# Kernel optimization log

Measured on AMD Instinct MI355X. Metric: run time of the kernel, lower is better.

Reference implementation:

```python
import jax, jax.numpy as jnp
import numpy as np

FP8_E4M3_MAX = 448.0  # torch.finfo(torch.float8_e4m3fn).max
TOKENS, D_IN, D_OUT = 8192, 4096, 4096


def setup_inputs() -> dict:
    key = jax.random.key(0)
    kx, kw, kb = jax.random.split(key, 3)
    x = jax.random.normal(kx, (TOKENS, D_IN), dtype=jnp.float32)
    # frozen bf16-like master weight, quantized to fp8 with per-tensor scale (as in __init__)
    w = jax.random.normal(kw, (D_OUT, D_IN), dtype=jnp.float32) * 0.02
    amax = jnp.abs(w).max()
    weight_scale = jnp.maximum(amax / FP8_E4M3_MAX, 1e-12).reshape(1)
    weight_fp8 = (w / weight_scale).astype(jnp.float8_e4m3fn)
    bias = jax.random.normal(kb, (D_OUT,), dtype=jnp.float32) * 0.01
    return {"x": x, "weight_fp8": weight_fp8, "weight_scale": weight_scale, "bias": bias}


def reference(x, weight_fp8, weight_scale, bias):
    # dequantize fp8 weight to activation dtype, scalar per-tensor scale
    w = weight_fp8.astype(x.dtype) * weight_scale.astype(x.dtype)  # [D_OUT, D_IN]
    return x @ w.T + bias  # [TOKENS, D_OUT]
```

## Files before the change

### kernel.cpp

```cpp
#include <hip/hip_runtime.h>


#define TILE 128
#define BKK  64
#define BM256 256
#define BN256 256

typedef __attribute__((ext_vector_type(8))) __bf16 bfrag8;
typedef __attribute__((ext_vector_type(4))) float  f32x4;
typedef __attribute__((ext_vector_type(8))) short  s8v;

#define GLOBAL_AS(p) ((const __attribute__((address_space(1))) void*)(p))
#define LDS_AS(p)    ((__attribute__((address_space(3))) void*)(p))

__device__ inline unsigned short f2bf(float f) {
    union { float f; unsigned u; } v; v.f = f;
    unsigned r = v.u + 0x7FFFu + ((v.u >> 16) & 1u);
    return (unsigned short)(r >> 16);
}
__device__ inline float bf2f(unsigned short u) {
    union { unsigned u; float f; } v; v.u = ((unsigned)u) << 16;
    return v.f;
}

__device__ inline int detect_w_f32(const void* w) {
    const unsigned short* u = (const unsigned short*)w;
    unsigned nz = 0;
#pragma unroll
    for (int i = 0; i < 64; ++i) nz |= u[2 * i];
    return nz == 0 ? 1 : 0;
}

__global__ void FP8FL_cvt_x(const float* __restrict__ x, short* __restrict__ xb, long n) {
    long i = ((long)blockIdx.x * blockDim.x + threadIdx.x) * 8;
    if (i >= n) return;
    float4 a = *(const float4*)(x + i);
    float4 b = *(const float4*)(x + i + 4);
    s8v r;
    r[0] = (short)f2bf(a.x); r[1] = (short)f2bf(a.y);
    r[2] = (short)f2bf(a.z); r[3] = (short)f2bf(a.w);
    r[4] = (short)f2bf(b.x); r[5] = (short)f2bf(b.y);
    r[6] = (short)f2bf(b.z); r[7] = (short)f2bf(b.w);
    *(s8v*)(xb + i) = r;
}

__global__ void FP8FL_cvt_w(const void* __restrict__ w, short* __restrict__ wb,
                            const float* __restrict__ scale_p, long n) {
    __shared__ int sdt;
    if (threadIdx.x == 0) sdt = detect_w_f32(w);
    __syncthreads();
    long i = ((long)blockIdx.x * blockDim.x + threadIdx.x) * 8;
    if (i >= n) return;
    const float s = scale_p[0];
    s8v r;
    if (sdt) {
        const float* wf = (const float*)w;
        float4 a = *(const float4*)(wf + i);
        float4 b = *(const float4*)(wf + i + 4);
        r[0] = (short)f2bf(a.x * s); r[1] = (short)f2bf(a.y * s);
        r[2] = (short)f2bf(a.z * s); r[3] = (short)f2bf(a.w * s);
        r[4] = (short)f2bf(b.x * s); r[5] = (short)f2bf(b.y * s);
        r[6] = (short)f2bf(b.z * s); r[7] = (short)f2bf(b.w * s);
    } else {
        const unsigned short* wu = (const unsigned short*)w;
        s8v v = *(const s8v*)(wu + i);
#pragma unroll
        for (int j = 0; j < 8; ++j)
            r[j] = (short)f2bf(bf2f((unsigned short)v[j]) * s);
    }
    *(s8v*)(wb + i) = r;
}

__device__ inline void stage_pair256(const short* __restrict__ A, const short* __restrict__ B,
                                     long row0, long col0, int K, int kc,
                                     char* __restrict__ lds, int d, int p,
                                     int wid, int lane) {
    char* Asl = lds + d * 65536 + p * 16384;
    char* Bsl = lds + d * 65536 + 32768 + p * 16384;
#pragma unroll
    for (int i = 0; i < 2; ++i) {
        int pc = i * 512 + wid * 64 + lane;
        int r  = pc >> 2;
        int j  = (pc & 3) ^ ((r >> 1) & 3);
        const short* ga = A + (size_t)(row0 + r) * K + kc + j * 8;
        const short* gb = B + (size_t)(col0 + r) * K + kc + j * 8;
        char* da = Asl + (i * 512 + wid * 64) * 16;
        char* db = Bsl + (i * 512 + wid * 64) * 16;
        __builtin_amdgcn_global_load_lds(GLOBAL_AS(ga), LDS_AS(da), 16, 0, 0);
        __builtin_amdgcn_global_load_lds(GLOBAL_AS(gb), LDS_AS(db), 16, 0, 0);
    }
}

__global__ __launch_bounds__(512, 2)
void FP8FL_gemm256(const short* __restrict__ A, const short* __restrict__ B,
                   const float* __restrict__ bias, float* __restrict__ C,
                   int M, int N, int K) {
    __shared__ char lds[131072];

    const int tid  = threadIdx.x;
    const int lane = tid & 63;
    const int wid  = tid >> 6;

    const int nwg = gridDim.x;
    const int bid = blockIdx.x;
    const int wg  = (nwg % 8 == 0) ? (bid % 8) * (nwg / 8) + (bid / 8) : bid;

    const int tiles_n = N / BN256;
    const long row0 = (long)(wg / tiles_n) * BM256;
    const long col0 = (long)(wg % tiles_n) * BN256;

    const int wm = wid >> 2, wn = wid & 3;
    const int rl = lane & 15, g = lane >> 4;

    f32x4 acc[8][4];
#pragma unroll
    for (int m = 0; m < 8; ++m)
#pragma unroll
        for (int n = 0; n < 4; ++n) acc[m][n] = (f32x4){0.f, 0.f, 0.f, 0.f};

    const int NT = K / BKK;

    stage_pair256(A, B, row0, col0, K, 0,  lds, 0, 0, wid, lane);
    stage_pair256(A, B, row0, col0, K, 32, lds, 0, 1, wid, lane);
    asm volatile("s_waitcnt vmcnt(4)" ::: "memory");
    __builtin_amdgcn_s_barrier();

    for (int t = 0; t < NT; ++t) {
        const int d = t & 1;
#pragma unroll
        for (int p = 0; p < 2; ++p) {
            const char* Asl = lds + d * 65536 + p * 16384;
            const char* Bsl = lds + d * 65536 + 32768 + p * 16384;
            bfrag8 af[8], bfv[4];
#pragma unroll
            for (int m = 0; m < 8; ++m) {
                int r  = wm * 128 + m * 16 + rl;
                int sl = g ^ ((r >> 1) & 3);
                af[m] = *(const bfrag8*)(Asl + (r * 4 + sl) * 16);
            }
#pragma unroll
            for (int n = 0; n < 4; ++n) {
                int r  = wn * 64 + n * 16 + rl;
                int sl = g ^ ((r >> 1) & 3);
                bfv[n] = *(const bfrag8*)(Bsl + (r * 4 + sl) * 16);
            }
            if (t + 1 < NT)
                stage_pair256(A, B, row0, col0, K, (t + 1) * BKK + p * 32,
                              lds, d ^ 1, p, wid, lane);

            __builtin_amdgcn_s_barrier();
            asm volatile("s_waitcnt lgkmcnt(0)" ::: "memory");
            __builtin_amdgcn_sched_barrier(0);
            __builtin_amdgcn_s_setprio(1);
#pragma unroll
            for (int m = 0; m < 8; ++m)
#pragma unroll
                for (int n = 0; n < 4; ++n)
                    acc[m][n] = __builtin_amdgcn_mfma_f32_16x16x32_bf16(af[m], bfv[n], acc[m][n], 0, 0, 0);
            __builtin_amdgcn_s_setprio(0);

            if (t + 1 < NT)      asm volatile("s_waitcnt vmcnt(4)" ::: "memory");
            else if (p == 0)     asm volatile("s_waitcnt vmcnt(0)" ::: "memory");
            __builtin_amdgcn_s_barrier();
        }
    }

    float bv[4];
#pragma unroll
    for (int n = 0; n < 4; ++n) bv[n] = bias[col0 + wn * 64 + n * 16 + rl];
#pragma unroll
    for (int m = 0; m < 8; ++m) {
#pragma unroll
        for (int jj = 0; jj < 4; ++jj) {
            long r = row0 + wm * 128 + m * 16 + g * 4 + jj;
            float* cp = C + r * (long)N + col0 + wn * 64 + rl;
#pragma unroll
            for (int n = 0; n < 4; ++n) cp[n * 16] = acc[m][n][jj] + bv[n];
        }
    }
}

__global__ void FP8FL_gemm(const short* __restrict__ A, const short* __restrict__ B,
                           const float* __restrict__ bias, float* __restrict__ C,
                           int M, int N, int K) {
    __shared__ short As[TILE * BKK];
    __shared__ short Bs[TILE * BKK];

    const int tid  = threadIdx.x;
    const int lane = tid & 63;
    const int wid  = tid >> 6;

    const int nwg = gridDim.x;
    const int bid = blockIdx.x;
    const int wg  = (nwg % 8 == 0) ? (bid % 8) * (nwg / 8) + (bid / 8) : bid;

    const int tiles_n = N / TILE;
    const int tm = wg / tiles_n, tn = wg % tiles_n;
    const long row0 = (long)tm * TILE;
    const long col0 = (long)tn * TILE;

    const int wm = wid >> 1, wn = wid & 1;

    f32x4 acc[4][4];
#pragma unroll
    for (int i = 0; i < 4; ++i)
#pragma unroll
        for (int j = 0; j < 4; ++j) acc[i][j] = (f32x4){0.f, 0.f, 0.f, 0.f};

    const int rl = lane & 15;
    const int g  = lane >> 4;

    for (int k0 = 0; k0 < K; k0 += BKK) {
        __syncthreads();
#pragma unroll
        for (int i = 0; i < 4; ++i) {
            int c  = i * 256 + tid;
            int r  = c >> 3;
            int ls = c & 7;
            const short* ga = A + ((size_t)(row0 + r) * K + k0 + ls * 8);
            const short* gb = B + ((size_t)(col0 + r) * K + k0 + ls * 8);
            int ldsoff = (i * 256 + wid * 64) * 16;
            __builtin_amdgcn_global_load_lds(GLOBAL_AS(ga), LDS_AS((char*)As + ldsoff), 16, 0, 0);
            __builtin_amdgcn_global_load_lds(GLOBAL_AS(gb), LDS_AS((char*)Bs + ldsoff), 16, 0, 0);
        }
        __syncthreads();

#pragma unroll
        for (int kk = 0; kk < 2; ++kk) {
            bfrag8 af[4], bfr[4];
            const int lsk = kk * 4 + g;
#pragma unroll
            for (int m = 0; m < 4; ++m) {
                int r  = wm * 64 + m * 16 + rl;
                af[m] = *(const bfrag8*)&As[r * 64 + lsk * 8];
            }
#pragma unroll
            for (int n = 0; n < 4; ++n) {
                int r  = wn * 64 + n * 16 + rl;
                bfr[n] = *(const bfrag8*)&Bs[r * 64 + lsk * 8];
            }
#pragma unroll
            for (int m = 0; m < 4; ++m)
#pragma unroll
                for (int n = 0; n < 4; ++n)
                    acc[m][n] = __builtin_amdgcn_mfma_f32_16x16x32_bf16(af[m], bfr[n], acc[m][n], 0, 0, 0);
        }
    }

    float bv[4];
#pragma unroll
    for (int n = 0; n < 4; ++n) bv[n] = bias[col0 + wn * 64 + n * 16 + rl];
#pragma unroll
    for (int m = 0; m < 4; ++m) {
#pragma unroll
        for (int j = 0; j < 4; ++j) {
            long r = row0 + wm * 64 + m * 16 + g * 4 + j;
            float* cp = C + r * (long)N + col0 + wn * 64 + rl;
#pragma unroll
            for (int n = 0; n < 4; ++n) cp[n * 16] = acc[m][n][j] + bv[n];
        }
    }
}

__global__ void FP8FL_gemm_fused(const float* __restrict__ X, const void* __restrict__ W,
                                 const float* __restrict__ scale_p,
                                 const float* __restrict__ bias, float* __restrict__ C,
                                 int M, int N, int K) {
    __shared__ short As[TILE * BKK];
    __shared__ short Bs[TILE * BKK];
    __shared__ int sdt;

    const int tid  = threadIdx.x;
    const int lane = tid & 63;
    const int wid  = tid >> 6;

    if (tid == 0) sdt = detect_w_f32(W);
    __syncthreads();
    const int wdt = sdt;
    const float s = scale_p[0];

    const int nwg = gridDim.x;
    const int bid = blockIdx.x;
    const int wg  = (nwg % 8 == 0) ? (bid % 8) * (nwg / 8) + (bid / 8) : bid;

    const int tiles_n = N / TILE;
    const long row0 = (long)(wg / tiles_n) * TILE;
    const long col0 = (long)(wg % tiles_n) * TILE;

    const int wm = wid >> 1, wn = wid & 1;

    f32x4 acc[4][4];
#pragma unroll
    for (int i = 0; i < 4; ++i)
#pragma unroll
        for (int j = 0; j < 4; ++j) acc[i][j] = (f32x4){0.f, 0.f, 0.f, 0.f};

    const int rl = lane & 15;
    const int g  = lane >> 4;

    for (int k0 = 0; k0 < K; k0 += BKK) {
        s8v va[4], vb[4];
#pragma unroll
        for (int i = 0; i < 4; ++i) {
            int c  = i * 256 + tid;
            int r  = c >> 3;
            int ls = c & 7;
            {
                const float* xp = X + ((size_t)(row0 + r) * K + k0 + ls * 8);
                float4 a = *(const float4*)xp;
                float4 b = *(const float4*)(xp + 4);
                s8v t;
                t[0] = (short)f2bf(a.x); t[1] = (short)f2bf(a.y);
                t[2] = (short)f2bf(a.z); t[3] = (short)f2bf(a.w);
                t[4] = (short)f2bf(b.x); t[5] = (short)f2bf(b.y);
                t[6] = (short)f2bf(b.z); t[7] = (short)f2bf(b.w);
                va[i] = t;
            }
            {
                size_t off = (size_t)(col0 + r) * K + k0 + ls * 8;
                s8v t;
                if (wdt) {
                    const float* wp = (const float*)W + off;
                    float4 a = *(const float4*)wp;
                    float4 b = *(const float4*)(wp + 4);
                    t[0] = (short)f2bf(a.x * s); t[1] = (short)f2bf(a.y * s);
                    t[2] = (short)f2bf(a.z * s); t[3] = (short)f2bf(a.w * s);
                    t[4] = (short)f2bf(b.x * s); t[5] = (short)f2bf(b.y * s);
                    t[6] = (short)f2bf(b.z * s); t[7] = (short)f2bf(b.w * s);
                } else {
                    const unsigned short* wp = (const unsigned short*)W + off;
                    s8v v = *(const s8v*)wp;
#pragma unroll
                    for (int j = 0; j < 8; ++j)
                        t[j] = (short)f2bf(bf2f((unsigned short)v[j]) * s);
                }
                vb[i] = t;
            }
        }
        __syncthreads();
#pragma unroll
        for (int i = 0; i < 4; ++i) {
            int c = i * 256 + tid;
            *(s8v*)((char*)As + (size_t)c * 16) = va[i];
            *(s8v*)((char*)Bs + (size_t)c * 16) = vb[i];
        }
        __syncthreads();

#pragma unroll
        for (int kk = 0; kk < 2; ++kk) {
            bfrag8 af[4], bfr[4];
            const int lsk = kk * 4 + g;
#pragma unroll
            for (int m = 0; m < 4; ++m) {
                int r  = wm * 64 + m * 16 + rl;
                af[m] = *(const bfrag8*)&As[r * 64 + lsk * 8];
            }
#pragma unroll
            for (int n = 0; n < 4; ++n) {
                int r  = wn * 64 + n * 16 + rl;
                bfr[n] = *(const bfrag8*)&Bs[r * 64 + lsk * 8];
            }
#pragma unroll
            for (int m = 0; m < 4; ++m)
#pragma unroll
                for (int n = 0; n < 4; ++n)
                    acc[m][n] = __builtin_amdgcn_mfma_f32_16x16x32_bf16(af[m], bfr[n], acc[m][n], 0, 0, 0);
        }
    }

    float bv[4];
#pragma unroll
    for (int n = 0; n < 4; ++n) bv[n] = bias[col0 + wn * 64 + n * 16 + rl];
#pragma unroll
    for (int m = 0; m < 4; ++m) {
#pragma unroll
        for (int j = 0; j < 4; ++j) {
            long r = row0 + wm * 64 + m * 16 + g * 4 + j;
            float* cp = C + r * (long)N + col0 + wn * 64 + rl;
#pragma unroll
            for (int n = 0; n < 4; ++n) cp[n * 16] = acc[m][n][j] + bv[n];
        }
    }
}

__global__ void FP8FL_naive(const float* __restrict__ x, const void* __restrict__ w,
                            const float* __restrict__ scale_p, const float* __restrict__ bias,
                            float* __restrict__ out, int M, int N, int K) {
    __shared__ int sdt;
    if (threadIdx.x == 0) sdt = detect_w_f32(w);
    __syncthreads();
    long o = (long)blockIdx.x * blockDim.x + threadIdx.x;
    if (o >= (long)M * N) return;
    int m = (int)(o / N), n = (int)(o % N);
    const float* xr = x + (size_t)m * K;
    float acc = 0.f;
    if (sdt) {
        const float* wr = (const float*)w + (size_t)n * K;
        for (int k = 0; k < K; ++k) acc += xr[k] * wr[k];
    } else {
        const unsigned short* wr = (const unsigned short*)w + (size_t)n * K;
        for (int k = 0; k < K; ++k) acc += xr[k] * bf2f(wr[k]);
    }
    out[o] = acc * scale_p[0] + bias[n];
}

extern "C" void kernel_launch(void* const* d_in, const int* in_sizes, int n_in,
                              void* d_out, int out_size, void* d_ws, size_t ws_size,
                              hipStream_t stream) {
    const float* x     = (const float*)d_in[0];
    const void*  w     = d_in[1];
    const float* scale = (const float*)d_in[2];
    const float* bias  = (const float*)d_in[3];
    float*       out   = (float*)d_out;

    const int N = in_sizes[3];
    const int K = in_sizes[1] / N;
    const int M = in_sizes[0] / K;

    const size_t need = (size_t)M * K * 2 + (size_t)N * K * 2;
    const bool ws_ok   = ws_size >= need;
    const bool dims256 = (M % BM256 == 0) && (N % BN256 == 0) && (K % BKK == 0);
    const bool dims128 = (M % TILE == 0) && (N % TILE == 0) && (K % BKK == 0);

    if (ws_ok && (dims256 || dims128)) {
        short* xb = (short*)d_ws;
        short* wb = (short*)((char*)d_ws + (size_t)M * K * 2);
        long nx = (long)M * K;
        long nw = (long)N * K;
        FP8FL_cvt_x<<<(int)((nx / 8 + 255) / 256), 256, 0, stream>>>(x, xb, nx);
        FP8FL_cvt_w<<<(int)((nw / 8 + 255) / 256), 256, 0, stream>>>(w, wb, scale, nw);
        if (dims256) {
            int grid = (M / BM256) * (N / BN256);
            FP8FL_gemm256<<<grid, 512, 0, stream>>>(xb, wb, bias, out, M, N, K);
        } else {
            int grid = (M / TILE) * (N / TILE);
            FP8FL_gemm<<<grid, 256, 0, stream>>>(xb, wb, bias, out, M, N, K);
        }
    } else if (dims128) {
        int grid = (M / TILE) * (N / TILE);
        FP8FL_gemm_fused<<<grid, 256, 0, stream>>>(x, w, scale, bias, out, M, N, K);
    } else {
        long total = (long)M * N;
        FP8FL_naive<<<(int)((total + 255) / 256), 256, 0, stream>>>(x, w, scale, bias, out, M, N, K);
    }
}
```

Before: 295.1 us.

## Restructure 256x256 GEMM pipeline to stage full K-tile per iteration

Replaces the two half-tile (p=0/1) staging and compute phases per K-step with a single phase. All A/B fragments for both halves are read from LDS first, then the whole next 64-wide K tile is prefetched, followed by 64 MFMAs and one __syncthreads. Fine-grained vmcnt waits and sched_barrier are replaced by plain barriers. This halves the barrier count but doubles the fragment registers, and the full drain at __syncthreads may expose global-load latency.

```diff
diff --git a/kernel.cpp b/kernel.cpp
--- a/kernel.cpp
+++ b/kernel.cpp
@@ -71,23 +71,26 @@
     *(s8v*)(wb + i) = r;
 }
 
-__device__ inline void stage_pair256(const short* __restrict__ A, const short* __restrict__ B,
+__device__ inline void stage_tile256(const short* __restrict__ A, const short* __restrict__ B,
                                      long row0, long col0, int K, int kc,
-                                     char* __restrict__ lds, int d, int p,
-                                     int wid, int lane) {
-    char* Asl = lds + d * 65536 + p * 16384;
-    char* Bsl = lds + d * 65536 + 32768 + p * 16384;
-#pragma unroll
-    for (int i = 0; i < 2; ++i) {
-        int pc = i * 512 + wid * 64 + lane;
-        int r  = pc >> 2;
-        int j  = (pc & 3) ^ ((r >> 1) & 3);
-        const short* ga = A + (size_t)(row0 + r) * K + kc + j * 8;
-        const short* gb = B + (size_t)(col0 + r) * K + kc + j * 8;
-        char* da = Asl + (i * 512 + wid * 64) * 16;
-        char* db = Bsl + (i * 512 + wid * 64) * 16;
-        __builtin_amdgcn_global_load_lds(GLOBAL_AS(ga), LDS_AS(da), 16, 0, 0);
-        __builtin_amdgcn_global_load_lds(GLOBAL_AS(gb), LDS_AS(db), 16, 0, 0);
+                                     char* __restrict__ lds, int d, int wid, int lane) {
+#pragma unroll
+    for (int p = 0; p < 2; ++p) {
+        char* Asl = lds + d * 65536 + p * 16384;
+        char* Bsl = lds + d * 65536 + 32768 + p * 16384;
+        int kk = kc + p * 32;
+#pragma unroll
+        for (int i = 0; i < 2; ++i) {
+            int pc = i * 512 + wid * 64 + lane;
+            int r  = pc >> 2;
+            int j  = (pc & 3) ^ ((r >> 1) & 3);
+            const short* ga = A + (size_t)(row0 + r) * K + kk + j * 8;
+            const short* gb = B + (size_t)(col0 + r) * K + kk + j * 8;
+            char* da = Asl + (i * 512 + wid * 64) * 16;
+            char* db = Bsl + (i * 512 + wid * 64) * 16;
+            __builtin_amdgcn_global_load_lds(GLOBAL_AS(ga), LDS_AS(da), 16, 0, 0);
+            __builtin_amdgcn_global_load_lds(GLOBAL_AS(gb), LDS_AS(db), 16, 0, 0);
+        }
     }
 }
 
@@ -120,49 +123,46 @@
 
     const int NT = K / BKK;
 
-    stage_pair256(A, B, row0, col0, K, 0,  lds, 0, 0, wid, lane);
-    stage_pair256(A, B, row0, col0, K, 32, lds, 0, 1, wid, lane);
-    asm volatile("s_waitcnt vmcnt(4)" ::: "memory");
-    __builtin_amdgcn_s_barrier();
+    stage_tile256(A, B, row0, col0, K, 0, lds, 0, wid, lane);
+    __syncthreads();
 
     for (int t = 0; t < NT; ++t) {
         const int d = t & 1;
+        const char* base = lds + d * 65536;
+
+        bfrag8 af[2][8], bf[2][4];
 #pragma unroll
         for (int p = 0; p < 2; ++p) {
-            const char* Asl = lds + d * 65536 + p * 16384;
-            const char* Bsl = lds + d * 65536 + 32768 + p * 16384;
-            bfrag8 af[8], bfv[4];
+            const char* Asl = base + p * 16384;
+            const char* Bsl = base + 32768 + p * 16384;
 #pragma unroll
             for (int m = 0; m < 8; ++m) {
                 int r  = wm * 128 + m * 16 + rl;
                 int sl = g ^ ((r >> 1) & 3);
-                af[m] = *(const bfrag8*)(Asl + (r * 4 + sl) * 16);
+                af[p][m] = *(const bfrag8*)(Asl + (r * 4 + sl) * 16);
             }
 #pragma unroll
             for (int n = 0; n < 4; ++n) {
                 int r  = wn * 64 + n * 16 + rl;
                 int sl = g ^ ((r >> 1) & 3);
-                bfv[n] = *(const bfrag8*)(Bsl + (r * 4 + sl) * 16);
-            }
-            if (t + 1 < NT)
-                stage_pair256(A, B, row0, col0, K, (t + 1) * BKK + p * 32,
-                              lds, d ^ 1, p, wid, lane);
-
-            __builtin_amdgcn_s_barrier();
-            asm volatile("s_waitcnt lgkmcnt(0)" ::: "memory");
-            __builtin_amdgcn_sched_barrier(0);
-            __builtin_amdgcn_s_setprio(1);
+                bf[p][n] = *(const bfrag8*)(Bsl + (r * 4 + sl) * 16);
+            }
+        }
+
+        if (t + 1 < NT)
+            stage_tile256(A, B, row0, col0, K, (t + 1) * BKK, lds, d ^ 1, wid, lane);
+
+        __builtin_amdgcn_s_setprio(1);
+#pragma unroll
+        for (int p = 0; p < 2; ++p)
 #pragma unroll
             for (int m = 0; m < 8; ++m)
 #pragma unroll
                 for (int n = 0; n < 4; ++n)
-                    acc[m][n] = __builtin_amdgcn_mfma_f32_16x16x32_bf16(af[m], bfv[n], acc[m][n], 0, 0, 0);
-            __builtin_amdgcn_s_setprio(0);
-
-            if (t + 1 < NT)      asm volatile("s_waitcnt vmcnt(4)" ::: "memory");
-            else if (p == 0)     asm volatile("s_waitcnt vmcnt(0)" ::: "memory");
-            __builtin_amdgcn_s_barrier();
-        }
+                    acc[m][n] = __builtin_amdgcn_mfma_f32_16x16x32_bf16(af[p][m], bf[p][n], acc[m][n], 0, 0, 0);
+        __builtin_amdgcn_s_setprio(0);
+
+        __syncthreads();
     }
 
     float bv[4];
@@ -195,9 +195,8 @@
     const int wg  = (nwg % 8 == 0) ? (bid % 8) * (nwg / 8) + (bid / 8) : bid;
 
     const int tiles_n = N / TILE;
-    const int tm = wg / tiles_n, tn = wg % tiles_n;
-    const long row0 = (long)tm * TILE;
-    const long col0 = (long)tn * TILE;
+    const long row0 = (long)(wg / tiles_n) * TILE;
+    const long col0 = (long)(wg % tiles_n) * TILE;
 
     const int wm = wid >> 1, wn = wid & 1;
 
```

Measured after the change: 273.3 us (median of 2 runs). 7.4% less time.

## Replace double-buffered LDS with 3-stage ring buffer and single barrier per K-step

Applied to the files above, without the earlier changes.

The 256x256 GEMM's LDS staging changes from two 64-wide K buffers, each split into two 32-wide halves, to a three-slot ring of 32-wide K tiles. Loads are issued two tiles ahead, and each iteration uses one barrier instead of two. This cuts LDS from 128KB to 96KB and removes a synchronization point per 32-K slice, aiming for better overlap of global loads with MFMA. The risk is a correctness race: the stage for t+2 is issued before the current slot's fragment reads, with no barrier at the top of the iteration. It targets slot (t+2)%3, which equals (t-1)%3, so it relies on the previous iteration's end barrier to ensure all waves have finished reading that slot.

```diff
diff --git a/kernel.cpp b/kernel.cpp
--- a/kernel.cpp
+++ b/kernel.cpp
@@ -3,6 +3,7 @@
 
 #define TILE 128
 #define BKK  64
+#define BK32 32
 #define BM256 256
 #define BN256 256
 
@@ -71,12 +72,11 @@
     *(s8v*)(wb + i) = r;
 }
 
-__device__ inline void stage_pair256(const short* __restrict__ A, const short* __restrict__ B,
-                                     long row0, long col0, int K, int kc,
-                                     char* __restrict__ lds, int d, int p,
-                                     int wid, int lane) {
-    char* Asl = lds + d * 65536 + p * 16384;
-    char* Bsl = lds + d * 65536 + 32768 + p * 16384;
+__device__ inline void stage_tile3(const short* __restrict__ A, const short* __restrict__ B,
+                                   long row0, long col0, int K, int kc,
+                                   char* __restrict__ lds, int s, int wid, int lane) {
+    char* Asl = lds + s * 32768;
+    char* Bsl = Asl + 16384;
 #pragma unroll
     for (int i = 0; i < 2; ++i) {
         int pc = i * 512 + wid * 64 + lane;
@@ -95,7 +95,7 @@
 void FP8FL_gemm256(const short* __restrict__ A, const short* __restrict__ B,
                    const float* __restrict__ bias, float* __restrict__ C,
                    int M, int N, int K) {
-    __shared__ char lds[131072];
+    __shared__ char lds[3 * 32768];
 
     const int tid  = threadIdx.x;
     const int lane = tid & 63;
@@ -118,51 +118,50 @@
 #pragma unroll
         for (int n = 0; n < 4; ++n) acc[m][n] = (f32x4){0.f, 0.f, 0.f, 0.f};
 
-    const int NT = K / BKK;
-
-    stage_pair256(A, B, row0, col0, K, 0,  lds, 0, 0, wid, lane);
-    stage_pair256(A, B, row0, col0, K, 32, lds, 0, 1, wid, lane);
+    const int NT = K / BK32;
+
+    stage_tile3(A, B, row0, col0, K, 0,    lds, 0, wid, lane);
+    stage_tile3(A, B, row0, col0, K, BK32, lds, 1, wid, lane);
     asm volatile("s_waitcnt vmcnt(4)" ::: "memory");
     __builtin_amdgcn_s_barrier();
-
+    __builtin_amdgcn_sched_barrier(0);
+
+    int scur = 0, snxt = 2;
     for (int t = 0; t < NT; ++t) {
-        const int d = t & 1;
-#pragma unroll
-        for (int p = 0; p < 2; ++p) {
-            const char* Asl = lds + d * 65536 + p * 16384;
-            const char* Bsl = lds + d * 65536 + 32768 + p * 16384;
-            bfrag8 af[8], bfv[4];
-#pragma unroll
-            for (int m = 0; m < 8; ++m) {
-                int r  = wm * 128 + m * 16 + rl;
-                int sl = g ^ ((r >> 1) & 3);
-                af[m] = *(const bfrag8*)(Asl + (r * 4 + sl) * 16);
-            }
-#pragma unroll
-            for (int n = 0; n < 4; ++n) {
-                int r  = wn * 64 + n * 16 + rl;
-                int sl = g ^ ((r >> 1) & 3);
-                bfv[n] = *(const bfrag8*)(Bsl + (r * 4 + sl) * 16);
-            }
-            if (t + 1 < NT)
-                stage_pair256(A, B, row0, col0, K, (t + 1) * BKK + p * 32,
-                              lds, d ^ 1, p, wid, lane);
-
-            __builtin_amdgcn_s_barrier();
-            asm volatile("s_waitcnt lgkmcnt(0)" ::: "memory");
-            __builtin_amdgcn_sched_barrier(0);
-            __builtin_amdgcn_s_setprio(1);
-#pragma unroll
-            for (int m = 0; m < 8; ++m)
-#pragma unroll
-                for (int n = 0; n < 4; ++n)
-                    acc[m][n] = __builtin_amdgcn_mfma_f32_16x16x32_bf16(af[m], bfv[n], acc[m][n], 0, 0, 0);
-            __builtin_amdgcn_s_setprio(0);
-
-            if (t + 1 < NT)      asm volatile("s_waitcnt vmcnt(4)" ::: "memory");
-            else if (p == 0)     asm volatile("s_waitcnt vmcnt(0)" ::: "memory");
-            __builtin_amdgcn_s_barrier();
-        }
+        if (t + 2 < NT)
+            stage_tile3(A, B, row0, col0, K, (t + 2) * BK32, lds, snxt, wid, lane);
+
+        const char* Asl = lds + scur * 32768;
+        const char* Bsl = Asl + 16384;
+        bfrag8 af[8], bf[4];
+#pragma unroll
+        for (int m = 0; m < 8; ++m) {
+            int r  = wm * 128 + m * 16 + rl;
+            int sl = g ^ ((r >> 1) & 3);
+            af[m] = *(const bfrag8*)(Asl + (r * 4 + sl) * 16);
+        }
+#pragma unroll
+        for (int n = 0; n < 4; ++n) {
+            int r  = wn * 64 + n * 16 + rl;
+            int sl = g ^ ((r >> 1) & 3);
+            bf[n] = *(const bfrag8*)(Bsl + (r * 4 + sl) * 16);
+        }
+
+        __builtin_amdgcn_s_setprio(1);
+#pragma unroll
+        for (int m = 0; m < 8; ++m)
+#pragma unroll
+            for (int n = 0; n < 4; ++n)
+                acc[m][n] = __builtin_amdgcn_mfma_f32_16x16x32_bf16(af[m], bf[n], acc[m][n], 0, 0, 0);
+        __builtin_amdgcn_s_setprio(0);
+
+        if (t + 2 < NT) asm volatile("s_waitcnt vmcnt(4)" ::: "memory");
+        else            asm volatile("s_waitcnt vmcnt(0)" ::: "memory");
+        __builtin_amdgcn_s_barrier();
+        __builtin_amdgcn_sched_barrier(0);
+
+        scur = (scur == 2) ? 0 : scur + 1;
+        snxt = (snxt == 2) ? 0 : snxt + 1;
     }
 
     float bv[4];
@@ -195,9 +194,8 @@
     const int wg  = (nwg % 8 == 0) ? (bid % 8) * (nwg / 8) + (bid / 8) : bid;
 
     const int tiles_n = N / TILE;
-    const int tm = wg / tiles_n, tn = wg % tiles_n;
-    const long row0 = (long)tm * TILE;
-    const long col0 = (long)tn * TILE;
+    const long row0 = (long)(wg / tiles_n) * TILE;
+    const long col0 = (long)(wg % tiles_n) * TILE;
 
     const int wm = wid >> 1, wn = wid & 1;
 
@@ -419,7 +417,7 @@
 
     const size_t need = (size_t)M * K * 2 + (size_t)N * K * 2;
     const bool ws_ok   = ws_size >= need;
-    const bool dims256 = (M % BM256 == 0) && (N % BN256 == 0) && (K % BKK == 0);
+    const bool dims256 = (M % BM256 == 0) && (N % BN256 == 0) && (K % BKK == 0) && (K / BK32 >= 4);
     const bool dims128 = (M % TILE == 0) && (N % TILE == 0) && (K % BKK == 0);
 
     if (ws_ok && (dims256 || dims128)) {
```

Result: no change. 291.5 us (-1.2%).
